# Performance work log

Measured on AMD Instinct MI355X. Metric: run time of the kernel, lower is better.

The kernel has to match this reference:

```python
import jax, jax.numpy as jnp
import numpy as np
from functools import partial

D = 512      # world_state_dim
M = 1000     # memory_size
H = 8        # attention heads
DH = D // H  # head dim
EPS = 1e-5


def _layernorm(x, g, b):
    mu = jnp.mean(x, axis=-1, keepdims=True)
    var = jnp.mean((x - mu) ** 2, axis=-1, keepdims=True)
    return (x - mu) * jax.lax.rsqrt(var + EPS) * g + b


def setup_inputs() -> dict:
    key = jax.random.key(0)
    ks = jax.random.split(key, 24)
    B = 8192
    w = lambda k, shp: (jax.random.normal(k, shp, dtype=jnp.float32) * 0.02)
    inp = {
        "observations": jax.random.normal(ks[0], (B, D), dtype=jnp.float32),
        "ego_motion": jax.random.normal(ks[1], (B, 16), dtype=jnp.float32),
        "world_memory": jax.random.normal(ks[2], (M, D), dtype=jnp.float32) * 0.1,
        # encoder: Linear(D,D) -> ReLU -> LN(D) -> Linear(D,D)
        "enc_w1": w(ks[3], (D, D)), "enc_b1": jnp.zeros((D,), jnp.float32),
        "enc_g": jnp.ones((D,), jnp.float32), "enc_beta": jnp.zeros((D,), jnp.float32),
        "enc_w2": w(ks[4], (D, D)), "enc_b2": jnp.zeros((D,), jnp.float32),
        # multihead attention in/out projections
        "wq": w(ks[5], (D, D)), "bq": jnp.zeros((D,), jnp.float32),
        "wk": w(ks[6], (D, D)), "bk": jnp.zeros((D,), jnp.float32),
        "wv": w(ks[7], (D, D)), "bv": jnp.zeros((D,), jnp.float32),
        "wo": w(ks[8], (D, D)), "bo": jnp.zeros((D,), jnp.float32),
        # transition: Linear(D+16,D) -> ReLU -> LN(D) -> Linear(D,D)
        "tr_w1": w(ks[9], (D, D + 16)), "tr_b1": jnp.zeros((D,), jnp.float32),
        "tr_g": jnp.ones((D,), jnp.float32), "tr_beta": jnp.zeros((D,), jnp.float32),
        "tr_w2": w(ks[10], (D, D)), "tr_b2": jnp.zeros((D,), jnp.float32),
        # quality head: Linear(D,128) -> ReLU -> Linear(128,1) -> Sigmoid
        "q_w1": w(ks[11], (128, D)), "q_b1": jnp.zeros((128,), jnp.float32),
        "q_w2": w(ks[12], (1, 128)), "q_b2": jnp.zeros((1,), jnp.float32),
        # random slots for memory-bank scatter-EMA update (replaces torch.randint)
        "update_indices": jax.random.randint(ks[13], (B,), 0, M, dtype=jnp.int32),
    }
    return inp


def _forward_core(observations, ego_motion, world_memory,
                  enc_w1, enc_b1, enc_g, enc_beta, enc_w2, enc_b2,
                  wq, bq, wk, bk, wv, bv, wo, bo,
                  tr_w1, tr_b1, tr_g, tr_beta, tr_w2, tr_b2,
                  q_w1, q_b1, q_w2, q_b2):
    B = observations.shape[0]
    # world_encoder
    h = jax.nn.relu(observations @ enc_w1.T + enc_b1)
    encoded = _layernorm(h, enc_g, enc_beta) @ enc_w2.T + enc_b2  # [B, D]
    # cross-attention: one query per batch row over shared memory bank
    q = (encoded @ wq.T + bq).reshape(B, H, DH)
    k = (world_memory @ wk.T + bk).reshape(M, H, DH)  # shared across batch
    v = (world_memory @ wv.T + bv).reshape(M, H, DH)
    scores = jnp.einsum("bhd,mhd->bhm", q, k) / jnp.sqrt(jnp.float32(DH))
    attn = jax.nn.softmax(scores, axis=-1)              # [B, H, M]
    ctx = jnp.einsum("bhm,mhd->bhd", attn, v).reshape(B, D)
    memory_states = ctx @ wo.T + bo
    # fuse + transition
    fused = 0.7 * encoded + 0.3 * memory_states
    x = jnp.concatenate([fused, ego_motion], axis=-1)   # [B, D+16]
    h2 = jax.nn.relu(x @ tr_w1.T + tr_b1)
    next_state = _layernorm(h2, tr_g, tr_beta) @ tr_w2.T + tr_b2  # [B, D]
    # quality head
    qh = jax.nn.relu(next_state @ q_w1.T + q_b1)
    quality = jax.nn.sigmoid(qh @ q_w2.T + q_b2)        # [B, 1]
    mem_weights = jnp.mean(attn, axis=1)                # [B, M] avg over heads
    return next_state, quality, mem_weights


def _update_memory_bank(world_memory, next_state, quality, update_indices):
    # Sequential scatter-EMA, faithful to the torch loop (duplicates compound).
    mask = quality[:, 0] > 0.7

    def step(mem, inp):
        idx, st, m = inp
        row = mem[idx]
        new_row = jnp.where(m, 0.9 * row + 0.1 * st, row)
        return mem.at[idx].set(new_row), None

    updated, _ = jax.lax.scan(step, world_memory, (update_indices, next_state, mask))
    return updated


@jax.jit
def reference(observations, ego_motion, world_memory,
              enc_w1, enc_b1, enc_g, enc_beta, enc_w2, enc_b2,
              wq, bq, wk, bk, wv, bv, wo, bo,
              tr_w1, tr_b1, tr_g, tr_beta, tr_w2, tr_b2,
              q_w1, q_b1, q_w2, q_b2, update_indices):
    next_state, quality, mem_weights = _forward_core(
        observations, ego_motion, world_memory,
        enc_w1, enc_b1, enc_g, enc_beta, enc_w2, enc_b2,
        wq, bq, wk, bk, wv, bv, wo, bo,
        tr_w1, tr_b1, tr_g, tr_beta, tr_w2, tr_b2,
        q_w1, q_b1, q_w2, q_b2)
    updated_memory = _update_memory_bank(world_memory, next_state, quality, update_indices)
    return next_state, quality, updated_memory
```

## Files before the change

### kernel.cpp

```cpp
#include <hip/hip_runtime.h>

#define B_ 8192
#define D_ 512
#define M_ 1000
#define H_ 8
#define LOG2E 1.4426950408889634f

typedef unsigned short u16;
typedef __attribute__((ext_vector_type(8))) short bf16x8;
typedef __attribute__((ext_vector_type(4))) float f32x4;

__device__ __forceinline__ float bf2f(u16 u) {
    union { unsigned u; float f; } c; c.u = ((unsigned)u) << 16; return c.f;
}
__device__ __forceinline__ u16 f2bf(float f) {
    union { float f; unsigned u; } c; c.f = f;
    unsigned r = (c.u + 0x7fffu + ((c.u >> 16) & 1u)) >> 16;
    return (u16)r;
}
__device__ __forceinline__ unsigned f2bf_fast_u(float f) {
    union { float f; unsigned u; } c; c.f = f;
    return (c.u + 0x8000u) >> 16;
}
__device__ __forceinline__ float wave_sum(float v) {
#pragma unroll
    for (int off = 32; off > 0; off >>= 1) v += __shfl_xor(v, off);
    return v;
}

template<bool RELU, bool WF32, bool VTOUT>
__device__ __forceinline__ void gemm_core(
    const u16* __restrict__ A0, const u16* __restrict__ A1,
    const u16* __restrict__ A2, int lda0, int lda1, int lda2,
    const u16* __restrict__ W0, const u16* __restrict__ W1,
    const u16* __restrict__ W2, int ldw0, int ldw1, int ldw2,
    int kb1, int kb2,
    const float* __restrict__ bias, float bscale, float cscale,
    float* __restrict__ Cf, u16* __restrict__ Cb, u16* __restrict__ VT,
    int M, int N, int K, int ldc)
{
    const int m0 = blockIdx.y * 64, n0 = blockIdx.x * 64;
    if (m0 >= M || n0 >= N) return;
    __shared__ u16 As[64 * 64];
    __shared__ u16 Bs[64 * 64];
    const int t = threadIdx.x, w = t >> 6, l = t & 63;
    const int wm = (w >> 1) * 32, wn = (w & 1) * 32;
    const int li = l & 15, quad = l >> 4;

    f32x4 acc[2][2];
#pragma unroll
    for (int i = 0; i < 2; ++i)
#pragma unroll
        for (int j = 0; j < 2; ++j) acc[i][j] = (f32x4){0.f, 0.f, 0.f, 0.f};

    for (int k0 = 0; k0 < K; k0 += 64) {
        const u16* Ab; const u16* Wb; int ldab, ldwb, ko;
        if (k0 < kb1)      { Ab = A0; ldab = lda0; Wb = W0; ldwb = ldw0; ko = k0; }
        else if (k0 < kb2) { Ab = A1; ldab = lda1; Wb = W1; ldwb = ldw1; ko = k0 - kb1; }
        else               { Ab = A2; ldab = lda2; Wb = W2; ldwb = ldw2; ko = k0 - kb2; }
#pragma unroll
        for (int i = 0; i < 2; ++i) {
            const int rl = w * 16 + i * 8 + (l >> 3);
            const int ck = (l & 7) ^ (rl & 7);
            int ga = m0 + rl; ga = ga < M ? ga : M - 1;
            __builtin_amdgcn_global_load_lds(
                (const __attribute__((address_space(1))) void*)(Ab + (size_t)ga * ldab + ko + ck * 8),
                (__attribute__((address_space(3))) void*)(As + (w * 16 + i * 8) * 64),
                16, 0, 0);
        }
#pragma unroll
        for (int i = 0; i < 2; ++i) {
            const int rl = w * 16 + i * 8 + (l >> 3);
            const int ck = (l & 7) ^ (rl & 7);
            int gb = n0 + rl; gb = gb < N ? gb : N - 1;
            __builtin_amdgcn_global_load_lds(
                (const __attribute__((address_space(1))) void*)(Wb + (size_t)gb * ldwb + ko + ck * 8),
                (__attribute__((address_space(3))) void*)(Bs + (w * 16 + i * 8) * 64),
                16, 0, 0);
        }
        __syncthreads();
#pragma unroll
        for (int ks = 0; ks < 2; ++ks) {
            const int ch = ks * 4 + quad;
            bf16x8 af[2], bfr[2];
#pragma unroll
            for (int mt = 0; mt < 2; ++mt) {
                const int r = wm + mt * 16 + li;
                af[mt] = *(const bf16x8*)(As + r * 64 + ((ch ^ (r & 7)) * 8));
            }
#pragma unroll
            for (int nt = 0; nt < 2; ++nt) {
                const int r = wn + nt * 16 + li;
                bfr[nt] = *(const bf16x8*)(Bs + r * 64 + ((ch ^ (r & 7)) * 8));
            }
#pragma unroll
            for (int mt = 0; mt < 2; ++mt)
#pragma unroll
                for (int nt = 0; nt < 2; ++nt)
                    acc[mt][nt] = __builtin_amdgcn_mfma_f32_16x16x32_bf16(
                        af[mt], bfr[nt], acc[mt][nt], 0, 0, 0);
        }
        __syncthreads();
    }

    float bv[2];
#pragma unroll
    for (int nt = 0; nt < 2; ++nt) bv[nt] = bias[n0 + wn + nt * 16 + li] * bscale;
#pragma unroll
    for (int mt = 0; mt < 2; ++mt) {
        const int row0 = m0 + wm + mt * 16 + quad * 4;
#pragma unroll
        for (int nt = 0; nt < 2; ++nt) {
            const int col = n0 + wn + nt * 16 + li;
            if (VTOUT && col >= 512) {
                ushort4 pk;
                u16 pv[4];
#pragma unroll
                for (int r = 0; r < 4; ++r) {
                    float v = acc[mt][nt][r] * cscale + bv[nt];
                    pv[r] = (row0 + r < M_) ? f2bf(v) : (u16)0;
                }
                pk.x = pv[0]; pk.y = pv[1]; pk.z = pv[2]; pk.w = pv[3];
                *(ushort4*)(VT + (size_t)(col - 512) * 1024 + row0) = pk;
            } else {
#pragma unroll
                for (int r = 0; r < 4; ++r) {
                    const int row = row0 + r;
                    if (row >= M) continue;
                    float v = acc[mt][nt][r] * cscale + bv[nt];
                    if (RELU) v = fmaxf(v, 0.f);
                    Cb[(size_t)row * ldc + col] = f2bf(v);
                    if (WF32) Cf[(size_t)row * ldc + col] = v;
                }
            }
        }
    }
}

template<bool RELU, bool WF32>
__launch_bounds__(256)
__global__ void mgemm(const u16* __restrict__ A0, const u16* __restrict__ A1,
                      const u16* __restrict__ A2, int lda0, int lda1, int lda2,
                      const u16* __restrict__ W0, const u16* __restrict__ W1,
                      const u16* __restrict__ W2, int ldw0, int ldw1, int ldw2,
                      int kb1, int kb2,
                      const float* __restrict__ bias, float bscale, float cscale,
                      float* __restrict__ Cf, u16* __restrict__ Cb,
                      int M, int N, int K, int ldc)
{
    gemm_core<RELU, WF32, false>(A0, A1, A2, lda0, lda1, lda2,
                                 W0, W1, W2, ldw0, ldw1, ldw2, kb1, kb2,
                                 bias, bscale, cscale, Cf, Cb, nullptr, M, N, K, ldc);
}

__launch_bounds__(256)
__global__ void foldgemm(const u16* __restrict__ w_q, const u16* __restrict__ w_tr1,
                         const u16* __restrict__ w_e2t, const u16* __restrict__ w_wot,
                         const float* __restrict__ zb,
                         u16* __restrict__ w_qe, u16* __restrict__ w_ae,
                         u16* __restrict__ w_co)
{
    const int z = blockIdx.z;
    if (z == 0)
        gemm_core<false, false, false>(w_q, w_q, w_q, 512, 512, 512,
            w_e2t, w_e2t, w_e2t, 512, 512, 512, 512, 512,
            zb, 0.f, 1.0f, nullptr, w_qe, nullptr, 512, 512, 512, 512);
    else if (z == 1)
        gemm_core<false, false, false>(w_tr1, w_tr1, w_tr1, 576, 576, 576,
            w_e2t, w_e2t, w_e2t, 512, 512, 512, 512, 512,
            zb, 0.f, 0.7f, nullptr, w_ae, nullptr, 512, 512, 512, 512);
    else
        gemm_core<false, false, false>(w_tr1, w_tr1, w_tr1, 576, 576, 576,
            w_wot, w_wot, w_wot, 512, 512, 512, 512, 512,
            zb, 0.f, 0.3f, nullptr, w_co, nullptr, 512, 512, 512, 512);
}

__launch_bounds__(256)
__global__ void qkvgemm(const u16* __restrict__ hn, const u16* __restrict__ w_qe,
                        const float* __restrict__ bqe, u16* __restrict__ qbuf,
                        const u16* __restrict__ wmem_bf, const u16* __restrict__ w_k,
                        const float* __restrict__ bkv, u16* __restrict__ KVbuf,
                        u16* __restrict__ VTb)
{
    if (blockIdx.z == 0)
        gemm_core<false, false, false>(hn, hn, hn, 512, 512, 512,
            w_qe, w_qe, w_qe, 512, 512, 512, 512, 512,
            bqe, 1.f, 1.f, nullptr, qbuf, nullptr, B_, 512, 512, 512);
    else
        gemm_core<false, false, true>(wmem_bf, wmem_bf, wmem_bf, 512, 512, 512,
            w_k, w_k, w_k, 512, 512, 512, 512, 512,
            bkv, 1.f, 1.f, nullptr, KVbuf, VTb, 1024, 1024, 512, 1024);
}

#define PADK 72

__launch_bounds__(256, 3)
__global__ void attn_kernel(const u16* __restrict__ Q, const u16* __restrict__ KV,
                            const u16* __restrict__ VT, u16* __restrict__ ctx)
{
    __shared__ u16 Ks[2][64 * 64];
    __shared__ u16 Vs[2][64 * 64];
    __shared__ u16 P[4 * 32 * PADK];
    const int t = threadIdx.x, w = t >> 6, l = t & 63;
    const int h = blockIdx.y;
    const int q0 = blockIdx.x * 128 + w * 32;
    u16* Pw = P + w * (32 * PADK);
    const int li = l & 15, quad = l >> 4;

    bf16x8 aq[2][2];
#pragma unroll
    for (int qnt = 0; qnt < 2; ++qnt)
#pragma unroll
        for (int ks = 0; ks < 2; ++ks) {
            const int row = q0 + qnt * 16 + li;
            aq[qnt][ks] = *(const bf16x8*)(Q + (size_t)row * 512 + h * 64 + ks * 32 + quad * 8);
        }

    bf16x8 ones;
#pragma unroll
    for (int i = 0; i < 8; ++i) ones[i] = (short)0x3F80;

    f32x4 oacc[2][4];
    f32x4 lacc[2];
#pragma unroll
    for (int mt = 0; mt < 2; ++mt) {
        lacc[mt] = (f32x4){0.f, 0.f, 0.f, 0.f};
#pragma unroll
        for (int nt = 0; nt < 4; ++nt) oacc[mt][nt] = (f32x4){0.f, 0.f, 0.f, 0.f};
    }

    auto stage = [&](int kc, int buf) {
#pragma unroll
        for (int i = 0; i < 2; ++i) {
            const int f = i * 256 + t;
            const int r = f >> 3;
            const int ck = (f & 7) ^ (r & 7);
            __builtin_amdgcn_global_load_lds(
                (const __attribute__((address_space(1))) void*)(KV + (size_t)(kc + r) * 1024 + h * 64 + ck * 8),
                (__attribute__((address_space(3))) void*)(&Ks[buf][f * 8]),
                16, 0, 0);
        }
#pragma unroll
        for (int i = 0; i < 2; ++i) {
            const int f = i * 256 + t;
            const int r = f >> 3;
            const int ck = (f & 7) ^ (r & 7);
            __builtin_amdgcn_global_load_lds(
                (const __attribute__((address_space(1))) void*)(VT + (size_t)(h * 64 + r) * 1024 + kc + ck * 8),
                (__attribute__((address_space(3))) void*)(&Vs[buf][f * 8]),
                16, 0, 0);
        }
    };

    stage(0, 0);
    for (int ic = 0; ic < 16; ++ic) {
        const int kc = ic * 64;
        __syncthreads();
        if (ic < 15) stage(kc + 64, (ic + 1) & 1);
        const u16* ksb = &Ks[ic & 1][0];
        const u16* vsb = &Vs[ic & 1][0];

        f32x4 s[4][2];
#pragma unroll
        for (int kmt = 0; kmt < 4; ++kmt)
#pragma unroll
            for (int qnt = 0; qnt < 2; ++qnt) s[kmt][qnt] = (f32x4){0.f, 0.f, 0.f, 0.f};
#pragma unroll
        for (int ks = 0; ks < 2; ++ks) {
            const int ch = ks * 4 + quad;
            bf16x8 bk[4];
#pragma unroll
            for (int kmt = 0; kmt < 4; ++kmt) {
                const int key = kmt * 16 + li;
                bk[kmt] = *(const bf16x8*)(ksb + key * 64 + ((ch ^ (key & 7)) * 8));
            }
#pragma unroll
            for (int kmt = 0; kmt < 4; ++kmt)
#pragma unroll
                for (int qnt = 0; qnt < 2; ++qnt)
                    s[kmt][qnt] = __builtin_amdgcn_mfma_f32_16x16x32_bf16(
                        bk[kmt], aq[qnt][ks], s[kmt][qnt], 0, 0, 0);
        }
        if (kc == 960) {
#pragma unroll
            for (int kmt = 2; kmt < 4; ++kmt)
#pragma unroll
                for (int r = 0; r < 4; ++r) {
                    const int key_local = kmt * 16 + quad * 4 + r;
                    if (960 + key_local >= M_) {
                        s[kmt][0][r] = -3.0e38f;
                        s[kmt][1][r] = -3.0e38f;
                    }
                }
        }
#pragma unroll
        for (int kmt = 0; kmt < 4; ++kmt)
#pragma unroll
            for (int qnt = 0; qnt < 2; ++qnt) {
                const unsigned b0 = f2bf_fast_u(exp2f(s[kmt][qnt][0]));
                const unsigned b1 = f2bf_fast_u(exp2f(s[kmt][qnt][1]));
                const unsigned b2w = f2bf_fast_u(exp2f(s[kmt][qnt][2]));
                const unsigned b3 = f2bf_fast_u(exp2f(s[kmt][qnt][3]));
                const int off = (qnt * 16 + li) * PADK + kmt * 16 + quad * 4;
                *(uint2*)(Pw + off) = make_uint2(b0 | (b1 << 16), b2w | (b3 << 16));
            }
#pragma unroll
        for (int ks = 0; ks < 2; ++ks) {
            const int ch = ks * 4 + quad;
            bf16x8 ap[2];
#pragma unroll
            for (int mt = 0; mt < 2; ++mt)
                ap[mt] = *(const bf16x8*)(Pw + (mt * 16 + li) * PADK + ch * 8);
#pragma unroll
            for (int mt = 0; mt < 2; ++mt)
                lacc[mt] = __builtin_amdgcn_mfma_f32_16x16x32_bf16(
                    ap[mt], ones, lacc[mt], 0, 0, 0);
#pragma unroll
            for (int nt = 0; nt < 4; ++nt) {
                const int dh = nt * 16 + li;
                const bf16x8 bvv = *(const bf16x8*)(vsb + dh * 64 + ((ch ^ (dh & 7)) * 8));
#pragma unroll
                for (int mt = 0; mt < 2; ++mt)
                    oacc[mt][nt] = __builtin_amdgcn_mfma_f32_16x16x32_bf16(
                        ap[mt], bvv, oacc[mt][nt], 0, 0, 0);
            }
        }
    }

#pragma unroll
    for (int mt = 0; mt < 2; ++mt)
#pragma unroll
        for (int r = 0; r < 4; ++r) {
            const int row = q0 + mt * 16 + quad * 4 + r;
            const float inv = 1.0f / lacc[mt][r];
#pragma unroll
            for (int nt = 0; nt < 4; ++nt)
                ctx[(size_t)row * 512 + h * 64 + nt * 16 + li] = f2bf(oacc[mt][nt][r] * inv);
        }
}

__launch_bounds__(256)
__global__ void ln_bf(u16* __restrict__ X, const float* __restrict__ g,
                      const float* __restrict__ be, int rows)
{
    const int row = blockIdx.x * 4 + (threadIdx.x >> 6);
    const int lane = threadIdx.x & 63;
    if (row >= rows) return;
    u16* p = X + (size_t)row * 512 + lane * 8;
    uint4 d = *(const uint4*)p;
    const unsigned dd[4] = {d.x, d.y, d.z, d.w};
    float v[8];
#pragma unroll
    for (int i = 0; i < 4; ++i) {
        v[2 * i]     = bf2f((u16)(dd[i] & 0xffffu));
        v[2 * i + 1] = bf2f((u16)(dd[i] >> 16));
    }
    float s = 0.f;
#pragma unroll
    for (int i = 0; i < 8; ++i) s += v[i];
    s = wave_sum(s);
    const float mu = s * (1.0f / 512.0f);
    float vs = 0.f;
#pragma unroll
    for (int i = 0; i < 8; ++i) { v[i] -= mu; vs += v[i] * v[i]; }
    vs = wave_sum(vs);
    const float r = rsqrtf(vs * (1.0f / 512.0f) + 1e-5f);
    const float* gp = g + lane * 8;
    const float* bp = be + lane * 8;
    unsigned o[4];
#pragma unroll
    for (int i = 0; i < 4; ++i) {
        const u16 lo = f2bf(v[2 * i] * r * gp[2 * i] + bp[2 * i]);
        const u16 hi = f2bf(v[2 * i + 1] * r * gp[2 * i + 1] + bp[2 * i + 1]);
        o[i] = (unsigned)lo | ((unsigned)hi << 16);
    }
    *(uint4*)p = make_uint4(o[0], o[1], o[2], o[3]);
}

__launch_bounds__(256)
__global__ void prep_all(const float* enc_w1, const float* wk_f, const float* wv_f,
                         const float* tr_w2, const float* q_w1, const float* wq,
                         const float* tr_w1, const float* enc_w2, const float* wo,
                         const float* obs, const float* wmem, const float* ego,
                         const float* bk, const float* bvv, const float* bq,
                         const float* enc_b2, const float* trb1, const float* bo,
                         u16* w_enc1, u16* w_k, u16* w_v, u16* w_tr2, u16* w_qh,
                         u16* w_q, u16* w_tr1, u16* w_e2t, u16* w_wot,
                         u16* obs_bf, u16* wmem_bf, u16* ego64,
                         float* bkv, float* bqe, float* btr)
{
    __shared__ float tl[64][65];
    const int seg = blockIdx.y;
    const int t = threadIdx.x;
    const int bx = blockIdx.x;

    if (seg <= 5) {
        const float* s; u16* d; int n; float sc = 1.0f;
        switch (seg) {
            case 0: s = enc_w1; d = w_enc1; n = 262144; break;
            case 1: s = wk_f;   d = w_k;    n = 262144; break;
            case 2: s = wv_f;   d = w_v;    n = 262144; break;
            case 3: s = tr_w2;  d = w_tr2;  n = 262144; break;
            case 4: s = q_w1;   d = w_qh;   n = 65536;  break;
            default: s = wq;    d = w_q;    n = 262144; sc = 0.125f * LOG2E; break;
        }
        const int i0 = (bx * 256 + t) * 4;
        if (i0 + 3 < n) {
            const float4 v = *(const float4*)(s + i0);
            ushort4 o;
            o.x = f2bf(v.x * sc); o.y = f2bf(v.y * sc);
            o.z = f2bf(v.z * sc); o.w = f2bf(v.w * sc);
            *(ushort4*)(d + i0) = o;
        }
    } else if (seg == 6) {
#pragma unroll
        for (int k = 0; k < 4; ++k) {
            const int i = (bx * 256 + t) * 4 + k;
            if (i < 294912) {
                const int r = i / 576, c = i - r * 576;
                w_tr1[i] = (c < 528) ? f2bf(tr_w1[r * 528 + c]) : (u16)0;
            }
        }
    } else if (seg <= 8) {
        if (bx >= 64) return;
        const float* S = (seg == 7) ? enc_w2 : wo;
        u16* D = (seg == 7) ? w_e2t : w_wot;
        const int r0 = (bx >> 3) * 64, c0 = (bx & 7) * 64;
#pragma unroll
        for (int i = 0; i < 16; ++i) {
            const int idx = t + i * 256;
            tl[idx >> 6][idx & 63] = S[(size_t)(r0 + (idx >> 6)) * 512 + c0 + (idx & 63)];
        }
        __syncthreads();
#pragma unroll
        for (int i = 0; i < 16; ++i) {
            const int idx = t + i * 256;
            const int c = idx >> 6, r = idx & 63;
            D[(size_t)(c0 + c) * 512 + r0 + r] = f2bf(tl[r][c]);
        }
    } else if (seg == 9) {
        const int nth = gridDim.x * 256;
        for (int i = bx * 256 + t; i < B_ * 512 / 4; i += nth) {
            const float4 v = ((const float4*)obs)[i];
            ushort4 o;
            o.x = f2bf(v.x); o.y = f2bf(v.y); o.z = f2bf(v.z); o.w = f2bf(v.w);
            ((ushort4*)obs_bf)[i] = o;
        }
    } else if (seg == 10) {
        const int nth = gridDim.x * 256;
        for (int i = bx * 256 + t; i < M_ * 512 / 4; i += nth) {
            const float4 v = ((const float4*)wmem)[i];
            ushort4 o;
            o.x = f2bf(v.x); o.y = f2bf(v.y); o.z = f2bf(v.z); o.w = f2bf(v.w);
            ((ushort4*)wmem_bf)[i] = o;
        }
    } else if (seg == 11) {
        const int nth = gridDim.x * 256;
        for (int i = bx * 256 + t; i < B_ * 64; i += nth) {
            const int b = i >> 6, j = i & 63;
            ego64[(size_t)b * 64 + j] = (j < 16) ? f2bf(ego[b * 16 + j]) : (u16)0;
        }
        const int tid = bx * 256 + t;
        if (tid < 1024) bkv[tid] = (tid < 512) ? bk[tid] : bvv[tid - 512];
    } else {
        if (bx >= 128) return;
        const int i = bx * 4 + (t >> 6);
        const int lane = t & 63;
        float s = 0.f;
        if (seg == 12) {
            const float* wr = wq + (size_t)i * 512 + lane * 8;
#pragma unroll
            for (int j = 0; j < 8; ++j) s += wr[j] * enc_b2[lane * 8 + j];
            s = wave_sum(s);
            if (lane == 0) bqe[i] = 0.125f * LOG2E * (bq[i] + s);
        } else {
            const float* wr = tr_w1 + (size_t)i * 528 + lane * 8;
#pragma unroll
            for (int j = 0; j < 8; ++j)
                s += wr[j] * (0.7f * enc_b2[lane * 8 + j] + 0.3f * bo[lane * 8 + j]);
            s = wave_sum(s);
            if (lane == 0) btr[i] = trb1[i] + s;
        }
    }
}

__global__ void quality_bf(const u16* __restrict__ qh, const float* __restrict__ w2,
                           const float* __restrict__ b2, float* __restrict__ outq,
                           int rows)
{
    const int row = blockIdx.x * 4 + (threadIdx.x >> 6);
    const int lane = threadIdx.x & 63;
    if (row >= rows) return;
    const u16* p = qh + (size_t)row * 128;
    float s = bf2f(p[lane]) * w2[lane] + bf2f(p[64 + lane]) * w2[64 + lane];
    s = wave_sum(s);
    if (lane == 0) outq[row] = 1.0f / (1.0f + expf(-(s + b2[0])));
}

__global__ void compact_kernel(const float* __restrict__ q,
                               int* __restrict__ list, int* __restrict__ cnt)
{
    __shared__ int wtot[16];
    __shared__ int sbase;
    const int t = threadIdx.x, w = t >> 6, lane = t & 63;
    if (t == 0) sbase = 0;
    __syncthreads();
    for (int c = 0; c < B_; c += 1024) {
        const int idx = c + t;
        const bool pred = (q[idx] > 0.7f);
        const unsigned long long bal = __ballot(pred);
        const int prefix = __popcll(bal & ((1ull << lane) - 1ull));
        if (lane == 0) wtot[w] = __popcll(bal);
        __syncthreads();
        int woff = 0;
        for (int i = 0; i < w; ++i) woff += wtot[i];
        if (pred) list[sbase + woff + prefix] = idx;
        __syncthreads();
        if (t == 0) {
            int tot = 0;
            for (int i = 0; i < 16; ++i) tot += wtot[i];
            sbase += tot;
        }
        __syncthreads();
    }
    if (t == 0) *cnt = sbase;
}

__global__ void update_memory_kernel(const float* __restrict__ mem,
                                     const float* __restrict__ ns,
                                     const int* __restrict__ upd,
                                     const int* __restrict__ list,
                                     const int* __restrict__ cnt,
                                     float* __restrict__ outmem)
{
    const int m = blockIdx.x;
    const int t = threadIdx.x;
    const int c4 = t * 4;
    float4 r = *(const float4*)(mem + (size_t)m * D_ + c4);
    const int n = *cnt;
    for (int i = 0; i < n; ++i) {
        const int b = list[i];
        if (upd[b] == m) {
            const float4 s = *(const float4*)(ns + (size_t)b * D_ + c4);
            r.x = 0.9f * r.x + 0.1f * s.x;
            r.y = 0.9f * r.y + 0.1f * s.y;
            r.z = 0.9f * r.z + 0.1f * s.z;
            r.w = 0.9f * r.w + 0.1f * s.w;
        }
    }
    *(float4*)(outmem + (size_t)m * D_ + c4) = r;
}

extern "C" void kernel_launch(void* const* d_in, const int* in_sizes, int n_in,
                              void* d_out, int out_size, void* d_ws, size_t ws_size,
                              hipStream_t stream)
{
    const float* obs    = (const float*)d_in[0];
    const float* ego    = (const float*)d_in[1];
    const float* wmem   = (const float*)d_in[2];
    const float* enc_w1 = (const float*)d_in[3];
    const float* enc_b1 = (const float*)d_in[4];
    const float* enc_g  = (const float*)d_in[5];
    const float* enc_be = (const float*)d_in[6];
    const float* enc_w2 = (const float*)d_in[7];
    const float* enc_b2 = (const float*)d_in[8];
    const float* wq = (const float*)d_in[9];
    const float* bq = (const float*)d_in[10];
    const float* wk_f = (const float*)d_in[11];
    const float* bk = (const float*)d_in[12];
    const float* wv_f = (const float*)d_in[13];
    const float* bvv = (const float*)d_in[14];
    const float* wo = (const float*)d_in[15];
    const float* bo = (const float*)d_in[16];
    const float* tr_w1 = (const float*)d_in[17];
    const float* tr_b1 = (const float*)d_in[18];
    const float* tr_g  = (const float*)d_in[19];
    const float* tr_be = (const float*)d_in[20];
    const float* tr_w2 = (const float*)d_in[21];
    const float* tr_b2 = (const float*)d_in[22];
    const float* q_w1 = (const float*)d_in[23];
    const float* q_b1 = (const float*)d_in[24];
    const float* q_w2 = (const float*)d_in[25];
    const float* q_b2 = (const float*)d_in[26];
    const int*   upd  = (const int*)d_in[27];

    float* out_ns  = (float*)d_out;
    float* out_q   = out_ns + (size_t)B_ * D_;
    float* out_mem = out_q + B_;

    u16* ws = (u16*)d_ws;
    size_t o = 0;
    u16* obs_bf  = ws + o; o += (size_t)B_ * 512;
    u16* wmem_bf = ws + o; o += (size_t)M_ * 512;
    u16* w_enc1  = ws + o; o += 262144;
    u16* w_k     = ws + o; o += 262144;
    u16* w_v     = ws + o; o += 262144;
    u16* w_tr2   = ws + o; o += 262144;
    u16* w_qh    = ws + o; o += 65536;
    u16* w_q     = ws + o; o += 262144;
    u16* w_tr1   = ws + o; o += (size_t)512 * 576;
    u16* w_e2t   = ws + o; o += 262144;
    u16* w_wot   = ws + o; o += 262144;
    u16* w_qe    = ws + o; o += 262144;
    u16* w_ae    = ws + o; o += 262144;
    u16* w_co    = ws + o; o += 262144;
    u16* hbuf    = ws + o; o += (size_t)B_ * 512;
    u16* qbuf    = ws + o; o += (size_t)B_ * 512;
    u16* KVbuf   = ws + o; o += (size_t)1024 * 1024;
    u16* VTb     = ws + o; o += (size_t)512 * 1024;
    u16* ctx     = ws + o; o += (size_t)B_ * 512;
    u16* h2b     = ws + o; o += (size_t)B_ * 512;
    u16* nsbf    = ws + o; o += (size_t)B_ * 512;
    u16* qhb     = ws + o; o += (size_t)B_ * 128;
    u16* ego64   = ws + o; o += (size_t)B_ * 64;
    float* bkv   = (float*)(ws + o); o += 2048;
    float* bqe   = (float*)(ws + o); o += 1024;
    float* btr   = (float*)(ws + o); o += 1024;
    int* list    = (int*)(ws + o);
    int* cnt     = list + B_;

    const dim3 blk(256);

    prep_all<<<dim3(576, 14), blk, 0, stream>>>(
        enc_w1, wk_f, wv_f, tr_w2, q_w1, wq, tr_w1, enc_w2, wo,
        obs, wmem, ego, bk, bvv, bq, enc_b2, tr_b1, bo,
        w_enc1, w_k, w_v, w_tr2, w_qh, w_q, w_tr1, w_e2t, w_wot,
        obs_bf, wmem_bf, ego64, bkv, bqe, btr);

    foldgemm<<<dim3(8, 8, 3), blk, 0, stream>>>(w_q, w_tr1, w_e2t, w_wot, bkv,
                                                w_qe, w_ae, w_co);

    mgemm<true, false><<<dim3(8, 128), blk, 0, stream>>>(
        obs_bf, obs_bf, obs_bf, 512, 512, 512, w_enc1, w_enc1, w_enc1, 512, 512, 512,
        512, 512, enc_b1, 1.f, 1.f, nullptr, hbuf, B_, 512, 512, 512);
    ln_bf<<<dim3(2048), blk, 0, stream>>>(hbuf, enc_g, enc_be, B_);

    qkvgemm<<<dim3(16, 128, 2), blk, 0, stream>>>(
        hbuf, w_qe, bqe, qbuf, wmem_bf, w_k, bkv, KVbuf, VTb);

    attn_kernel<<<dim3(64, 8), blk, 0, stream>>>(qbuf, KVbuf, VTb, ctx);

    mgemm<true, false><<<dim3(8, 128), blk, 0, stream>>>(
        hbuf, ctx, ego64, 512, 512, 64, w_ae, w_co, w_tr1 + 512, 512, 512, 576,
        512, 1024, btr, 1.f, 1.f, nullptr, h2b, B_, 512, 1088, 512);
    ln_bf<<<dim3(2048), blk, 0, stream>>>(h2b, tr_g, tr_be, B_);

    mgemm<false, true><<<dim3(8, 128), blk, 0, stream>>>(
        h2b, h2b, h2b, 512, 512, 512, w_tr2, w_tr2, w_tr2, 512, 512, 512,
        512, 512, tr_b2, 1.f, 1.f, out_ns, nsbf, B_, 512, 512, 512);

    mgemm<true, false><<<dim3(2, 128), blk, 0, stream>>>(
        nsbf, nsbf, nsbf, 512, 512, 512, w_qh, w_qh, w_qh, 512, 512, 512,
        512, 512, q_b1, 1.f, 1.f, nullptr, qhb, B_, 128, 512, 128);
    quality_bf<<<dim3(2048), blk, 0, stream>>>(qhb, q_w2, q_b2, out_q, B_);

    compact_kernel<<<dim3(1), dim3(1024), 0, stream>>>(out_q, list, cnt);
    update_memory_kernel<<<dim3(M_), dim3(128), 0, stream>>>(
        wmem, out_ns, upd, list, cnt, out_mem);
}
```

Measured before the change: 273.8 us.

## Double GEMM K-tile to 128 and merge encoder, KV, and weight-fold GEMMs

The GEMM core now stages 128-wide K tiles in shared memory, using a 16-chunk XOR swizzle, so each main-loop step does twice the MFMA work per barrier pair. The padded tr_w1 and ego buffers grow to a K-multiple of 128 to fit this. Separately, the encoder GEMM, memory K/V projection and the three weight-folding GEMMs are launched together as one kernel, removing a launch and letting independent work overlap. In exchange, the extra zero padding costs some wasted compute, the larger LDS footprint may reduce occupancy, and the merged kernel launches many idle blocks that return early.

```diff
diff --git a/kernel.cpp b/kernel.cpp
--- a/kernel.cpp
+++ b/kernel.cpp
@@ -41,8 +41,8 @@
 {
     const int m0 = blockIdx.y * 64, n0 = blockIdx.x * 64;
     if (m0 >= M || n0 >= N) return;
-    __shared__ u16 As[64 * 64];
-    __shared__ u16 Bs[64 * 64];
+    __shared__ u16 As[64 * 128];
+    __shared__ u16 Bs[64 * 128];
     const int t = threadIdx.x, w = t >> 6, l = t & 63;
     const int wm = (w >> 1) * 32, wn = (w & 1) * 32;
     const int li = l & 15, quad = l >> 4;
@@ -53,45 +53,47 @@
 #pragma unroll
         for (int j = 0; j < 2; ++j) acc[i][j] = (f32x4){0.f, 0.f, 0.f, 0.f};
 
-    for (int k0 = 0; k0 < K; k0 += 64) {
+    for (int k0 = 0; k0 < K; k0 += 128) {
         const u16* Ab; const u16* Wb; int ldab, ldwb, ko;
         if (k0 < kb1)      { Ab = A0; ldab = lda0; Wb = W0; ldwb = ldw0; ko = k0; }
         else if (k0 < kb2) { Ab = A1; ldab = lda1; Wb = W1; ldwb = ldw1; ko = k0 - kb1; }
         else               { Ab = A2; ldab = lda2; Wb = W2; ldwb = ldw2; ko = k0 - kb2; }
 #pragma unroll
-        for (int i = 0; i < 2; ++i) {
-            const int rl = w * 16 + i * 8 + (l >> 3);
-            const int ck = (l & 7) ^ (rl & 7);
+        for (int i = 0; i < 4; ++i) {
+            const int f = i * 256 + t;
+            const int rl = f >> 4;
+            const int ck = (f & 15) ^ (rl & 15);
             int ga = m0 + rl; ga = ga < M ? ga : M - 1;
             __builtin_amdgcn_global_load_lds(
                 (const __attribute__((address_space(1))) void*)(Ab + (size_t)ga * ldab + ko + ck * 8),
-                (__attribute__((address_space(3))) void*)(As + (w * 16 + i * 8) * 64),
+                (__attribute__((address_space(3))) void*)(As + f * 8),
                 16, 0, 0);
         }
 #pragma unroll
-        for (int i = 0; i < 2; ++i) {
-            const int rl = w * 16 + i * 8 + (l >> 3);
-            const int ck = (l & 7) ^ (rl & 7);
+        for (int i = 0; i < 4; ++i) {
+            const int f = i * 256 + t;
+            const int rl = f >> 4;
+            const int ck = (f & 15) ^ (rl & 15);
             int gb = n0 + rl; gb = gb < N ? gb : N - 1;
             __builtin_amdgcn_global_load_lds(
                 (const __attribute__((address_space(1))) void*)(Wb + (size_t)gb * ldwb + ko + ck * 8),
-                (__attribute__((address_space(3))) void*)(Bs + (w * 16 + i * 8) * 64),
+                (__attribute__((address_space(3))) void*)(Bs + f * 8),
                 16, 0, 0);
         }
         __syncthreads();
 #pragma unroll
-        for (int ks = 0; ks < 2; ++ks) {
+        for (int ks = 0; ks < 4; ++ks) {
             const int ch = ks * 4 + quad;
             bf16x8 af[2], bfr[2];
 #pragma unroll
             for (int mt = 0; mt < 2; ++mt) {
                 const int r = wm + mt * 16 + li;
-                af[mt] = *(const bf16x8*)(As + r * 64 + ((ch ^ (r & 7)) * 8));
+                af[mt] = *(const bf16x8*)(As + r * 128 + ((ch ^ (r & 15)) * 8));
             }
 #pragma unroll
             for (int nt = 0; nt < 2; ++nt) {
                 const int r = wn + nt * 16 + li;
-                bfr[nt] = *(const bf16x8*)(Bs + r * 64 + ((ch ^ (r & 7)) * 8));
+                bfr[nt] = *(const bf16x8*)(Bs + r * 128 + ((ch ^ (r & 15)) * 8));
             }
 #pragma unroll
             for (int mt = 0; mt < 2; ++mt)
@@ -154,42 +156,37 @@
 }
 
 __launch_bounds__(256)
-__global__ void foldgemm(const u16* __restrict__ w_q, const u16* __restrict__ w_tr1,
+__global__ void megagemm(const u16* __restrict__ obs_bf, const u16* __restrict__ w_enc1,
+                         const float* __restrict__ enc_b1, u16* __restrict__ hbuf,
+                         const u16* __restrict__ wmem_bf, const u16* __restrict__ w_k,
+                         const float* __restrict__ bkv, u16* __restrict__ KVbuf,
+                         u16* __restrict__ VTb,
+                         const u16* __restrict__ w_q, const u16* __restrict__ w_tr1,
                          const u16* __restrict__ w_e2t, const u16* __restrict__ w_wot,
-                         const float* __restrict__ zb,
                          u16* __restrict__ w_qe, u16* __restrict__ w_ae,
                          u16* __restrict__ w_co)
 {
     const int z = blockIdx.z;
     if (z == 0)
-        gemm_core<false, false, false>(w_q, w_q, w_q, 512, 512, 512,
-            w_e2t, w_e2t, w_e2t, 512, 512, 512, 512, 512,
-            zb, 0.f, 1.0f, nullptr, w_qe, nullptr, 512, 512, 512, 512);
+        gemm_core<true, false, false>(obs_bf, obs_bf, obs_bf, 512, 512, 512,
+            w_enc1, w_enc1, w_enc1, 512, 512, 512, 512, 512,
+            enc_b1, 1.f, 1.f, nullptr, hbuf, nullptr, B_, 512, 512, 512);
     else if (z == 1)
-        gemm_core<false, false, false>(w_tr1, w_tr1, w_tr1, 576, 576, 576,
-            w_e2t, w_e2t, w_e2t, 512, 512, 512, 512, 512,
-            zb, 0.f, 0.7f, nullptr, w_ae, nullptr, 512, 512, 512, 512);
-    else
-        gemm_core<false, false, false>(w_tr1, w_tr1, w_tr1, 576, 576, 576,
-            w_wot, w_wot, w_wot, 512, 512, 512, 512, 512,
-            zb, 0.f, 0.3f, nullptr, w_co, nullptr, 512, 512, 512, 512);
-}
-
-__launch_bounds__(256)
-__global__ void qkvgemm(const u16* __restrict__ hn, const u16* __restrict__ w_qe,
-                        const float* __restrict__ bqe, u16* __restrict__ qbuf,
-                        const u16* __restrict__ wmem_bf, const u16* __restrict__ w_k,
-                        const float* __restrict__ bkv, u16* __restrict__ KVbuf,
-                        u16* __restrict__ VTb)
-{
-    if (blockIdx.z == 0)
-        gemm_core<false, false, false>(hn, hn, hn, 512, 512, 512,
-            w_qe, w_qe, w_qe, 512, 512, 512, 512, 512,
-            bqe, 1.f, 1.f, nullptr, qbuf, nullptr, B_, 512, 512, 512);
-    else
         gemm_core<false, false, true>(wmem_bf, wmem_bf, wmem_bf, 512, 512, 512,
             w_k, w_k, w_k, 512, 512, 512, 512, 512,
             bkv, 1.f, 1.f, nullptr, KVbuf, VTb, 1024, 1024, 512, 1024);
+    else if (z == 2)
+        gemm_core<false, false, false>(w_q, w_q, w_q, 512, 512, 512,
+            w_e2t, w_e2t, w_e2t, 512, 512, 512, 512, 512,
+            bkv, 0.f, 1.0f, nullptr, w_qe, nullptr, 512, 512, 512, 512);
+    else if (z == 3)
+        gemm_core<false, false, false>(w_tr1, w_tr1, w_tr1, 640, 640, 640,
+            w_e2t, w_e2t, w_e2t, 512, 512, 512, 512, 512,
+            bkv, 0.f, 0.7f, nullptr, w_ae, nullptr, 512, 512, 512, 512);
+    else
+        gemm_core<false, false, false>(w_tr1, w_tr1, w_tr1, 640, 640, 640,
+            w_wot, w_wot, w_wot, 512, 512, 512, 512, 512,
+            bkv, 0.f, 0.3f, nullptr, w_co, nullptr, 512, 512, 512, 512);
 }
 
 #define PADK 72
@@ -413,13 +410,10 @@
             *(ushort4*)(d + i0) = o;
         }
     } else if (seg == 6) {
-#pragma unroll
-        for (int k = 0; k < 4; ++k) {
-            const int i = (bx * 256 + t) * 4 + k;
-            if (i < 294912) {
-                const int r = i / 576, c = i - r * 576;
-                w_tr1[i] = (c < 528) ? f2bf(tr_w1[r * 528 + c]) : (u16)0;
-            }
+        const int nth = gridDim.x * 256;
+        for (int i = bx * 256 + t; i < 512 * 640; i += nth) {
+            const int r = i / 640, c = i - r * 640;
+            w_tr1[i] = (c < 528) ? f2bf(tr_w1[r * 528 + c]) : (u16)0;
         }
     } else if (seg <= 8) {
         if (bx >= 64) return;
@@ -456,9 +450,9 @@
         }
     } else if (seg == 11) {
         const int nth = gridDim.x * 256;
-        for (int i = bx * 256 + t; i < B_ * 64; i += nth) {
-            const int b = i >> 6, j = i & 63;
-            ego64[(size_t)b * 64 + j] = (j < 16) ? f2bf(ego[b * 16 + j]) : (u16)0;
+        for (int i = bx * 256 + t; i < B_ * 128; i += nth) {
+            const int b = i >> 7, j = i & 127;
+            ego64[(size_t)b * 128 + j] = (j < 16) ? f2bf(ego[b * 16 + j]) : (u16)0;
         }
         const int tid = bx * 256 + t;
         if (tid < 1024) bkv[tid] = (tid < 512) ? bk[tid] : bvv[tid - 512];
@@ -598,7 +592,7 @@
     u16* w_tr2   = ws + o; o += 262144;
     u16* w_qh    = ws + o; o += 65536;
     u16* w_q     = ws + o; o += 262144;
-    u16* w_tr1   = ws + o; o += (size_t)512 * 576;
+    u16* w_tr1   = ws + o; o += (size_t)512 * 640;
     u16* w_e2t   = ws + o; o += 262144;
     u16* w_wot   = ws + o; o += 262144;
     u16* w_qe    = ws + o; o += 262144;
@@ -612,7 +606,7 @@
     u16* h2b     = ws + o; o += (size_t)B_ * 512;
     u16* nsbf    = ws + o; o += (size_t)B_ * 512;
     u16* qhb     = ws + o; o += (size_t)B_ * 128;
-    u16* ego64   = ws + o; o += (size_t)B_ * 64;
+    u16* ego64   = ws + o; o += (size_t)B_ * 128;
     float* bkv   = (float*)(ws + o); o += 2048;
     float* bqe   = (float*)(ws + o); o += 1024;
     float* btr   = (float*)(ws + o); o += 1024;
@@ -627,22 +621,21 @@
         w_enc1, w_k, w_v, w_tr2, w_qh, w_q, w_tr1, w_e2t, w_wot,
         obs_bf, wmem_bf, ego64, bkv, bqe, btr);
 
-    foldgemm<<<dim3(8, 8, 3), blk, 0, stream>>>(w_q, w_tr1, w_e2t, w_wot, bkv,
-                                                w_qe, w_ae, w_co);
+    megagemm<<<dim3(16, 128, 5), blk, 0, stream>>>(
+        obs_bf, w_enc1, enc_b1, hbuf, wmem_bf, w_k, bkv, KVbuf, VTb,
+        w_q, w_tr1, w_e2t, w_wot, w_qe, w_ae, w_co);
+
+    ln_bf<<<dim3(2048), blk, 0, stream>>>(hbuf, enc_g, enc_be, B_);
+
+    mgemm<false, false><<<dim3(8, 128), blk, 0, stream>>>(
+        hbuf, hbuf, hbuf, 512, 512, 512, w_qe, w_qe, w_qe, 512, 512, 512,
+        512, 512, bqe, 1.f, 1.f, nullptr, qbuf, B_, 512, 512, 512);
+
+    attn_kernel<<<dim3(64, 8), blk, 0, stream>>>(qbuf, KVbuf, VTb, ctx);
 
     mgemm<true, false><<<dim3(8, 128), blk, 0, stream>>>(
-        obs_bf, obs_bf, obs_bf, 512, 512, 512, w_enc1, w_enc1, w_enc1, 512, 512, 512,
-        512, 512, enc_b1, 1.f, 1.f, nullptr, hbuf, B_, 512, 512, 512);
-    ln_bf<<<dim3(2048), blk, 0, stream>>>(hbuf, enc_g, enc_be, B_);
-
-    qkvgemm<<<dim3(16, 128, 2), blk, 0, stream>>>(
-        hbuf, w_qe, bqe, qbuf, wmem_bf, w_k, bkv, KVbuf, VTb);
-
-    attn_kernel<<<dim3(64, 8), blk, 0, stream>>>(qbuf, KVbuf, VTb, ctx);
-
-    mgemm<true, false><<<dim3(8, 128), blk, 0, stream>>>(
-        hbuf, ctx, ego64, 512, 512, 64, w_ae, w_co, w_tr1 + 512, 512, 512, 576,
-        512, 1024, btr, 1.f, 1.f, nullptr, h2b, B_, 512, 1088, 512);
+        hbuf, ctx, ego64, 512, 512, 128, w_ae, w_co, w_tr1 + 512, 512, 512, 640,
+        512, 1024, btr, 1.f, 1.f, nullptr, h2b, B_, 512, 1152, 512);
     ln_bf<<<dim3(2048), blk, 0, stream>>>(h2b, tr_g, tr_be, B_);
 
     mgemm<false, true><<<dim3(8, 128), blk, 0, stream>>>(
```

Measured after the change: 303.2 us. 10.8% more time.
